# Kernel optimization log

Measured on AMD Instinct MI355X. Metric: run time of the kernel, lower is better.

The kernel has to match this reference:

```python
import jax, jax.numpy as jnp
import numpy as np

B, S, H, NH = 8, 1024, 1024, 16
HD = H // NH  # head dim = 64

def setup_inputs() -> dict:
    key = jax.random.key(0)
    ks = jax.random.split(key, 7)
    sc = 0.02
    return {
        "activation": jax.random.normal(ks[0], (B, S, H), jnp.float32),
        "qw": jax.random.normal(ks[1], (H, H), jnp.float32) * sc,
        "qb": jax.random.normal(ks[2], (H,), jnp.float32) * sc,
        "kw": jax.random.normal(ks[3], (H, H), jnp.float32) * sc,
        "kb": jax.random.normal(ks[4], (H,), jnp.float32) * sc,
        "vw": jax.random.normal(ks[5], (H, H), jnp.float32) * sc,
        "vb": jax.random.normal(ks[6], (H,), jnp.float32) * sc,
    }

def reference(activation, qw, qb, kw, kb, vw, vb):
    # QKV projections (torch Linear: x @ W^T + b)
    def proj(x, w, b):
        y = jnp.einsum('bsh,oh->bso', x, w) + b
        # split heads: [B,S,H] -> [B,NH,S,HD]
        return y.reshape(B, S, NH, HD).transpose(0, 2, 1, 3)
    q = proj(activation, qw, qb)
    k = proj(activation, kw, kb)
    v = proj(activation, vw, vb)
    # NOTE: source scales by 1/sqrt(hidden_dim), NOT 1/sqrt(head_dim)
    scale = 1.0 / jnp.sqrt(jnp.float32(H))
    scores = jnp.einsum('bnqd,bnkd->bnqk', q, k) * scale
    probs = jax.nn.softmax(scores, axis=-1)
    ctx = jnp.einsum('bnqk,bnkd->bnqd', probs, v)
    # merge heads: [B,NH,S,HD] -> [B,S,H]
    return ctx.transpose(0, 2, 1, 3).reshape(B, S, H)
```

## Files before the change

### kernel.cpp

```cpp
#include <hip/hip_runtime.h>
#include <cstdint>
#include <cstddef>

#define B_   8
#define S_   1024
#define H_   1024
#define NH_  16
#define HD_  64
#define M_   8192
#define N3_  3072
#define K_   1024

typedef __attribute__((ext_vector_type(8))) short bf16x8;
typedef __attribute__((ext_vector_type(4))) float f32x4;
typedef __attribute__((ext_vector_type(16))) float f32x16;
typedef __attribute__((ext_vector_type(8))) unsigned short u16x8;
typedef __attribute__((ext_vector_type(4))) unsigned u32x4;

__device__ __forceinline__ unsigned short f2bf(float f) {
  unsigned u = __builtin_bit_cast(unsigned, f);
  u += 0x7fffu + ((u >> 16) & 1u);
  return (unsigned short)(u >> 16);
}

__device__ __forceinline__ unsigned long long pack4bf(float a, float b,
                                                      float c, float d) {
  return (unsigned long long)f2bf(a)
       | ((unsigned long long)f2bf(b) << 16)
       | ((unsigned long long)f2bf(c) << 32)
       | ((unsigned long long)f2bf(d) << 48);
}

__device__ __forceinline__ unsigned cvtpk(float a, float b) {
  unsigned r;
  asm("v_cvt_pk_bf16_f32 %0, %1, %2" : "=v"(r) : "v"(a), "v"(b));
  return r;
}

__global__ void cvt_kernel(const float* __restrict__ src,
                           unsigned short* __restrict__ dst, int n) {
  const int stride = gridDim.x * blockDim.x * 8;
  for (int i = (blockIdx.x * blockDim.x + threadIdx.x) * 8; i < n; i += stride) {
    float4 a = *reinterpret_cast<const float4*>(src + i);
    float4 b = *reinterpret_cast<const float4*>(src + i + 4);
    u16x8 o;
    o[0] = f2bf(a.x); o[1] = f2bf(a.y); o[2] = f2bf(a.z); o[3] = f2bf(a.w);
    o[4] = f2bf(b.x); o[5] = f2bf(b.y); o[6] = f2bf(b.z); o[7] = f2bf(b.w);
    *reinterpret_cast<u16x8*>(dst + i) = o;
  }
}

__global__ void wcvt_kernel(const float* __restrict__ q,
                            const float* __restrict__ k,
                            const float* __restrict__ v,
                            unsigned short* __restrict__ dst) {
  const int i = (blockIdx.x * blockDim.x + threadIdx.x) * 8;
  const float* src;
  int off;
  if (i < 1048576)      { src = q; off = i; }
  else if (i < 2097152) { src = k; off = i - 1048576; }
  else                  { src = v; off = i - 2097152; }
  float4 a = *reinterpret_cast<const float4*>(src + off);
  float4 b = *reinterpret_cast<const float4*>(src + off + 4);
  u16x8 o;
  o[0] = f2bf(a.x); o[1] = f2bf(a.y); o[2] = f2bf(a.z); o[3] = f2bf(a.w);
  o[4] = f2bf(b.x); o[5] = f2bf(b.y); o[6] = f2bf(b.z); o[7] = f2bf(b.w);
  *reinterpret_cast<u16x8*>(dst + i) = o;
}

__global__ __launch_bounds__(256, 2) void qkv_gemm(
    const unsigned short* __restrict__ A,
    const unsigned short* __restrict__ Bw,
    const float* __restrict__ qb, const float* __restrict__ kb,
    const float* __restrict__ vb,
    unsigned short* __restrict__ Qh,
    unsigned short* __restrict__ Kh,
    unsigned short* __restrict__ Vth)
{
  extern __shared__ char sm[];
  const int t = threadIdx.x;
  const int lane = t & 63;
  const int wm = t >> 7, wn = (t >> 6) & 1;

  const int bid = blockIdx.x;
  const int c = bid >> 3;
  const int g = c >> 6;
  const int m = (c >> 3) & 7;
  const int n = c & 7;
  const int bm = (bid & 7) * 8 + m;
  const int bn = g * 8 + n;

  const char* Ab = (const char*)A + (size_t)bm * 128 * 2048;
  const char* Bb = (const char*)Bw + (size_t)bn * 128 * 2048;

  f32x4 acc[4][4] = {};

  #define STG(kt, buf)                                                         \
    { char* Ld = sm + (buf) * 32768;                                           \
      _Pragma("unroll")                                                        \
      for (int i = 0; i < 4; ++i) {                                            \
        const int off = (i * 256 + t) * 16;                                    \
        const int row = off >> 7;                                              \
        const int sc  = ((off >> 4) & 7) ^ (row & 7);                          \
        __builtin_amdgcn_global_load_lds(                                      \
          (const __attribute__((address_space(1))) void*)(Ab + (size_t)row * 2048 + (kt) * 128 + sc * 16), \
          (__attribute__((address_space(3))) void*)(Ld + off), 16, 0, 0);      \
        __builtin_amdgcn_global_load_lds(                                      \
          (const __attribute__((address_space(1))) void*)(Bb + (size_t)row * 2048 + (kt) * 128 + sc * 16), \
          (__attribute__((address_space(3))) void*)(Ld + 16384 + off), 16, 0, 0); \
      } }

  STG(0, 0)
  __syncthreads();

  for (int kt = 0; kt < 16; ++kt) {
    if (kt < 15) STG(kt + 1, (kt + 1) & 1)
    const char* Acur = sm + (kt & 1) * 32768;
    const char* Bcur = Acur + 16384;
    #pragma unroll
    for (int kk = 0; kk < 2; ++kk) {
      bf16x8 af[4], bf[4];
      #pragma unroll
      for (int mb = 0; mb < 4; ++mb) {
        const int row = wm * 64 + mb * 16 + (lane & 15);
        const int j   = kk * 4 + (lane >> 4);
        af[mb] = *(const bf16x8*)(Acur + row * 128 + ((j ^ (row & 7)) << 4));
      }
      #pragma unroll
      for (int nb = 0; nb < 4; ++nb) {
        const int row = wn * 64 + nb * 16 + (lane & 15);
        const int j   = kk * 4 + (lane >> 4);
        bf[nb] = *(const bf16x8*)(Bcur + row * 128 + ((j ^ (row & 7)) << 4));
      }
      __builtin_amdgcn_s_setprio(1);
      #pragma unroll
      for (int mb = 0; mb < 4; ++mb)
        #pragma unroll
        for (int nb = 0; nb < 4; ++nb)
          acc[mb][nb] = __builtin_amdgcn_mfma_f32_16x16x32_bf16(
              af[mb], bf[nb], acc[mb][nb], 0, 0, 0);
      __builtin_amdgcn_s_setprio(0);
    }
    __syncthreads();
  }

  const int tensor = bn >> 3;
  const float scl = (tensor == 0) ? 0.04508422f : 1.0f;
  const float* bias = (tensor == 0) ? qb : (tensor == 1) ? kb : vb;
  char* E = sm;
  const int bloc = bm >> 3;
  const int srow = (bm & 7) * 128;

  if (tensor < 2) {
    #pragma unroll
    for (int nb = 0; nb < 4; ++nb) {
      const int col = wn * 64 + nb * 16 + (lane & 15);
      const float bv = bias[(bn & 7) * 128 + col];
      #pragma unroll
      for (int mb = 0; mb < 4; ++mb) {
        #pragma unroll
        for (int r = 0; r < 4; ++r) {
          const int row = wm * 64 + mb * 16 + (lane >> 4) * 4 + r;
          const int byo = row * 256 + ((((col >> 3) ^ (row & 7)) << 4) | ((col & 7) << 1));
          *(unsigned short*)(E + byo) = f2bf((acc[mb][nb][r] + bv) * scl);
        }
      }
    }
    __syncthreads();
    unsigned short* dst = (tensor == 0) ? Qh : Kh;
    #pragma unroll
    for (int cch = 0; cch < 8; ++cch) {
      const int o = t * 128 + cch * 16;
      const int row = o >> 8;
      const int colb = o & 255;
      const int col = colb >> 1;
      u32x4 v = *(const u32x4*)(E + row * 256 + ((((colb >> 4) ^ (row & 7)) << 4)));
      const int sg = srow + row;
      const int nhh = (bn & 7) * 2 + (col >> 6);
      const size_t db = ((size_t)(bloc * NH_ + nhh) * S_ + sg) * 128 + (col & 63) * 2;
      *(u32x4*)((char*)dst + db) = v;
    }
  } else {
    #pragma unroll
    for (int nb = 0; nb < 4; ++nb) {
      const int col = wn * 64 + nb * 16 + (lane & 15);
      const float bv = bias[(bn & 7) * 128 + col];
      #pragma unroll
      for (int mb = 0; mb < 4; ++mb) {
        const int row0 = wm * 64 + mb * 16 + (lane >> 4) * 4;
        unsigned long long w = pack4bf(acc[mb][nb][0] + bv, acc[mb][nb][1] + bv,
                                       acc[mb][nb][2] + bv, acc[mb][nb][3] + bv);
        const int byo = col * 256 + ((((row0 >> 3) ^ (col & 7)) << 4) | ((row0 & 7) << 1));
        *(unsigned long long*)(E + byo) = w;
      }
    }
    __syncthreads();
    #pragma unroll
    for (int cch = 0; cch < 8; ++cch) {
      const int o = t * 128 + cch * 16;
      const int col = o >> 8;
      const int rowb = o & 255;
      const int row0 = rowb >> 1;
      u32x4 v = *(const u32x4*)(E + col * 256 + ((((rowb >> 4) ^ (col & 7)) << 4)));
      const int sg0 = srow + row0;
      const int nhh = (bn & 7) * 2 + (col >> 6);
      const size_t db = (size_t)(bloc * NH_ + nhh) * 131072 +
                        (size_t)(sg0 >> 6) * 8192 + (col & 63) * 128 + (sg0 & 63) * 2;
      *(u32x4*)((char*)Vth + db) = v;
    }
  }
}

__device__ __forceinline__ bf16x8 mk_frag(const f32x16& s, const int base) {
  unsigned a0 = cvtpk(s[base + 0], s[base + 1]);
  unsigned a1 = cvtpk(s[base + 2], s[base + 3]);
  unsigned b0 = cvtpk(s[base + 4], s[base + 5]);
  unsigned b1 = cvtpk(s[base + 6], s[base + 7]);
  asm("v_permlane32_swap_b32 %0, %1" : "+v"(a0), "+v"(b0));
  asm("v_permlane32_swap_b32 %0, %1" : "+v"(a1), "+v"(b1));
  u32x4 u = {a0, a1, b0, b1};
  return __builtin_bit_cast(bf16x8, u);
}

__global__ __launch_bounds__(256, 3) void attn_kernel(
    const unsigned short* __restrict__ Qh,
    const unsigned short* __restrict__ Kh,
    const unsigned short* __restrict__ Vth,
    float* __restrict__ Out)
{
  __shared__ char smx[2][16384];
  const int t = threadIdx.x;
  const int lane = t & 63;
  const int wave = t >> 6;
  const int l31 = lane & 31;
  const int hi = lane >> 5;
  const int hw = blockIdx.x;
  const int xcd = hw & 7;
  const int qt = (hw >> 3) & 7;
  const int bh = (hw >> 6) * 8 + xcd;
  const int b = bh >> 4, nh = bh & 15;

  const unsigned short* Qp = Qh + (size_t)bh * (S_ * HD_);
  const char* Kp = (const char*)Kh + (size_t)bh * 131072;
  const char* Vp = (const char*)Vth + (size_t)bh * 131072;
  const int q0 = qt * 128 + wave * 32;

  bf16x8 bq[4];
  #pragma unroll
  for (int st = 0; st < 4; ++st)
    bq[st] = *reinterpret_cast<const bf16x8*>(
        Qp + (size_t)(q0 + l31) * HD_ + st * 16 + hi * 8);

  const int soff0 = wave * 1024 + lane * 16;
  #define STAGE_TILE(dstbase, srcbase)                                            \
    _Pragma("unroll")                                                             \
    for (int j = 0; j < 2; ++j) {                                                 \
      const int off = j * 4096 + soff0;                                           \
      const int row = off >> 7;                                                   \
      const int sc  = ((off >> 4) & 7) ^ (row & 7);                               \
      __builtin_amdgcn_global_load_lds(                                           \
          (const __attribute__((address_space(1))) void*)((srcbase) + row * 128 + sc * 16), \
          (__attribute__((address_space(3))) void*)((dstbase) + off), 16, 0, 0);  \
    }

  STAGE_TILE(&smx[0][0],    Kp)
  STAGE_TILE(&smx[0][8192], Vp)
  __syncthreads();

  f32x16 o0 = {}, o1 = {};
  float lsum = 0.f;
  const int swr = l31 & 7;

  for (int kt = 0; kt < 16; ++kt) {
    const int cur = kt & 1;
    if (kt < 15) {
      STAGE_TILE(&smx[cur ^ 1][0],    Kp + (kt + 1) * 8192)
      STAGE_TILE(&smx[cur ^ 1][8192], Vp + (kt + 1) * 8192)
    }
    const char* Kb = &smx[cur][0];
    const char* Vb = &smx[cur][8192];

    f32x16 s0 = {}, s1 = {};
    #pragma unroll
    for (int st = 0; st < 4; ++st) {
      const int c = ((st * 2 + hi) ^ swr) << 4;
      bf16x8 ka = *reinterpret_cast<const bf16x8*>(Kb + l31 * 128 + c);
      bf16x8 kc = *reinterpret_cast<const bf16x8*>(Kb + (l31 + 32) * 128 + c);
      s0 = __builtin_amdgcn_mfma_f32_32x32x16_bf16(ka, bq[st], s0, 0, 0, 0);
      s1 = __builtin_amdgcn_mfma_f32_32x32x16_bf16(kc, bq[st], s1, 0, 0, 0);
    }

    bf16x8 va[4];
    #pragma unroll
    for (int ks = 0; ks < 2; ++ks) {
      const int c = ((ks * 2 + hi) ^ swr) << 4;
      va[ks * 2]     = *reinterpret_cast<const bf16x8*>(Vb + l31 * 128 + c);
      va[ks * 2 + 1] = *reinterpret_cast<const bf16x8*>(Vb + (l31 + 32) * 128 + c);
    }
    #pragma unroll
    for (int r = 0; r < 16; ++r) {
      s0[r] = __builtin_amdgcn_exp2f(s0[r]);
      lsum += s0[r];
    }
    bf16x8 f0 = mk_frag(s0, 0);
    bf16x8 f1 = mk_frag(s0, 8);
    o0 = __builtin_amdgcn_mfma_f32_32x32x16_bf16(f0, va[0], o0, 0, 0, 0);
    o1 = __builtin_amdgcn_mfma_f32_32x32x16_bf16(f0, va[1], o1, 0, 0, 0);
    o0 = __builtin_amdgcn_mfma_f32_32x32x16_bf16(f1, va[2], o0, 0, 0, 0);
    o1 = __builtin_amdgcn_mfma_f32_32x32x16_bf16(f1, va[3], o1, 0, 0, 0);

    #pragma unroll
    for (int ks = 0; ks < 2; ++ks) {
      const int c = (((ks + 2) * 2 + hi) ^ swr) << 4;
      va[ks * 2]     = *reinterpret_cast<const bf16x8*>(Vb + l31 * 128 + c);
      va[ks * 2 + 1] = *reinterpret_cast<const bf16x8*>(Vb + (l31 + 32) * 128 + c);
    }
    #pragma unroll
    for (int r = 0; r < 16; ++r) {
      s1[r] = __builtin_amdgcn_exp2f(s1[r]);
      lsum += s1[r];
    }
    bf16x8 f2 = mk_frag(s1, 0);
    bf16x8 f3 = mk_frag(s1, 8);
    o0 = __builtin_amdgcn_mfma_f32_32x32x16_bf16(f2, va[0], o0, 0, 0, 0);
    o1 = __builtin_amdgcn_mfma_f32_32x32x16_bf16(f2, va[1], o1, 0, 0, 0);
    o0 = __builtin_amdgcn_mfma_f32_32x32x16_bf16(f3, va[2], o0, 0, 0, 0);
    o1 = __builtin_amdgcn_mfma_f32_32x32x16_bf16(f3, va[3], o1, 0, 0, 0);

    __syncthreads();
  }

  const float ltot = lsum + __shfl_xor(lsum, 32);
  const float inv = 1.0f / ltot;
  #pragma unroll
  for (int r = 0; r < 16; ++r) {
    const int crow = (r & 3) + 8 * (r >> 2) + 4 * hi;
    const float invq = __shfl(inv, crow);
    float* op = Out + ((size_t)(b * S_ + q0 + crow)) * H_ + nh * HD_ + l31;
    op[0]  = o0[r] * invq;
    op[32] = o1[r] * invq;
  }
}

extern "C" void kernel_launch(void* const* d_in, const int* in_sizes, int n_in,
                              void* d_out, int out_size, void* d_ws, size_t ws_size,
                              hipStream_t stream) {
  const float* act = (const float*)d_in[0];
  const float* qw  = (const float*)d_in[1];
  const float* qb  = (const float*)d_in[2];
  const float* kw  = (const float*)d_in[3];
  const float* kb  = (const float*)d_in[4];
  const float* vw  = (const float*)d_in[5];
  const float* vb  = (const float*)d_in[6];

  char* ws = (char*)d_ws;
  unsigned short* actb = (unsigned short*)ws;
  unsigned short* wb   = (unsigned short*)(ws + 16777216);
  unsigned short* Qh   = (unsigned short*)(ws + 23068672);
  unsigned short* Kh   = Qh + 8388608;
  unsigned short* Vth  = Kh + 8388608;

  cvt_kernel<<<4096, 256, 0, stream>>>(act, actb, M_ * K_);
  wcvt_kernel<<<1536, 256, 0, stream>>>(qw, kw, vw, wb);

  hipFuncSetAttribute((const void*)qkv_gemm,
                      hipFuncAttributeMaxDynamicSharedMemorySize, 65536);
  qkv_gemm<<<1536, 256, 65536, stream>>>(actb, wb, qb, kb, vb, Qh, Kh, Vth);

  attn_kernel<<<1024, 256, 0, stream>>>(Qh, Kh, Vth, (float*)d_out);
}
```

Before: 122.7 us.

## Enlarge QKV GEMM tile to 256x128 with 512 threads and triple-buffered LDS

The QKV projection GEMM now runs 8 waves per block on a 256x128 output tile instead of 4 waves on 128x128. This halves the block count and improves reuse of the weight tile loaded into LDS. The main loop switches to a three-stage LDS ring, 144 KB in total, with two tiles prefetched ahead. A and B loads are issued in separate k-phases and synchronised with explicit vmcnt waits and raw barriers instead of __syncthreads. The epilogue indexing is adapted to the taller tile. The cost is one block per CU, so latency hiding depends on the hand-written pipeline rather than on occupancy.

Measured after the change: 129.9 us. 5.8% more time.

```diff
diff --git a/kernel.cpp b/kernel.cpp
--- a/kernel.cpp
+++ b/kernel.cpp
@@ -68,7 +68,7 @@
   *reinterpret_cast<u16x8*>(dst + i) = o;
 }
 
-__global__ __launch_bounds__(256, 2) void qkv_gemm(
+__global__ __launch_bounds__(512, 1) void qkv_gemm(
     const unsigned short* __restrict__ A,
     const unsigned short* __restrict__ Bw,
     const float* __restrict__ qb, const float* __restrict__ kb,
@@ -80,76 +80,107 @@
   extern __shared__ char sm[];
   const int t = threadIdx.x;
   const int lane = t & 63;
-  const int wm = t >> 7, wn = (t >> 6) & 1;
+  const int wave = t >> 6;
+  const int wm = wave >> 1;
+  const int wn = wave & 1;
 
   const int bid = blockIdx.x;
   const int c = bid >> 3;
-  const int g = c >> 6;
-  const int m = (c >> 3) & 7;
+  const int g = c >> 5;
+  const int m = (c >> 3) & 3;
   const int n = c & 7;
-  const int bm = (bid & 7) * 8 + m;
+  const int bm = (bid & 7) * 4 + m;
   const int bn = g * 8 + n;
 
-  const char* Ab = (const char*)A + (size_t)bm * 128 * 2048;
+  const char* Ab = (const char*)A + (size_t)bm * 256 * 2048;
   const char* Bb = (const char*)Bw + (size_t)bn * 128 * 2048;
 
   f32x4 acc[4][4] = {};
 
-  #define STG(kt, buf)                                                         \
-    { char* Ld = sm + (buf) * 32768;                                           \
+  #define STGA(kt, q, h)                                                       \
+    { char* Ld = sm + (q) * 49152 + (h) * 16384;                               \
       _Pragma("unroll")                                                        \
-      for (int i = 0; i < 4; ++i) {                                            \
-        const int off = (i * 256 + t) * 16;                                    \
-        const int row = off >> 7;                                              \
+      for (int j = 0; j < 2; ++j) {                                            \
+        const int off = j * 8192 + t * 16;                                     \
+        const int row = (h) * 128 + (off >> 7);                                \
         const int sc  = ((off >> 4) & 7) ^ (row & 7);                          \
         __builtin_amdgcn_global_load_lds(                                      \
           (const __attribute__((address_space(1))) void*)(Ab + (size_t)row * 2048 + (kt) * 128 + sc * 16), \
           (__attribute__((address_space(3))) void*)(Ld + off), 16, 0, 0);      \
+      } }
+  #define STGB(kt, q)                                                          \
+    { char* Ld = sm + (q) * 49152 + 32768;                                     \
+      _Pragma("unroll")                                                        \
+      for (int j = 0; j < 2; ++j) {                                            \
+        const int off = j * 8192 + t * 16;                                     \
+        const int row = off >> 7;                                              \
+        const int sc  = ((off >> 4) & 7) ^ (row & 7);                          \
         __builtin_amdgcn_global_load_lds(                                      \
           (const __attribute__((address_space(1))) void*)(Bb + (size_t)row * 2048 + (kt) * 128 + sc * 16), \
-          (__attribute__((address_space(3))) void*)(Ld + 16384 + off), 16, 0, 0); \
+          (__attribute__((address_space(3))) void*)(Ld + off), 16, 0, 0);      \
       } }
 
-  STG(0, 0)
+  #define VM6 asm volatile("s_waitcnt vmcnt(6)" ::: "memory")
+  #define VM0 asm volatile("s_waitcnt vmcnt(0)" ::: "memory")
+  #define BARR asm volatile("s_barrier" ::: "memory")
+
+  #define PH_READS(KK)                                                         \
+    bf16x8 af[4], bf[4];                                                       \
+    _Pragma("unroll")                                                          \
+    for (int mb = 0; mb < 4; ++mb) {                                           \
+      const int row = wm * 64 + mb * 16 + (lane & 15);                         \
+      af[mb] = *(const bf16x8*)(Acur + row * 128 +                             \
+                ((((KK) * 4 + (lane >> 4)) ^ (row & 7)) << 4));                \
+    }                                                                          \
+    _Pragma("unroll")                                                          \
+    for (int nb = 0; nb < 4; ++nb) {                                           \
+      const int row = wn * 64 + nb * 16 + (lane & 15);                         \
+      bf[nb] = *(const bf16x8*)(Bcur + row * 128 +                             \
+                ((((KK) * 4 + (lane >> 4)) ^ (row & 7)) << 4));                \
+    }
+  #define PH_MFMA                                                              \
+    __builtin_amdgcn_s_setprio(1);                                             \
+    _Pragma("unroll")                                                          \
+    for (int mb = 0; mb < 4; ++mb)                                             \
+      _Pragma("unroll")                                                        \
+      for (int nb = 0; nb < 4; ++nb)                                           \
+        acc[mb][nb] = __builtin_amdgcn_mfma_f32_16x16x32_bf16(                 \
+            af[mb], bf[nb], acc[mb][nb], 0, 0, 0);                             \
+    __builtin_amdgcn_s_setprio(0);
+
+  STGA(0, 0, 0) STGA(0, 0, 1) STGB(0, 0)
+  STGA(1, 1, 0) STGA(1, 1, 1) STGB(1, 1)
+  VM6;
+  BARR;
+
+  for (int kt = 0; kt < 16; ++kt) {
+    const char* Acur = sm + (kt % 3) * 49152;
+    const char* Bcur = Acur + 32768;
+    const int qn = (kt + 2) % 3;
+    {
+      PH_READS(0)
+      if (kt < 14) { STGA(kt + 2, qn, 0) STGA(kt + 2, qn, 1) }
+      BARR;
+      PH_MFMA
+      BARR;
+    }
+    {
+      PH_READS(1)
+      if (kt < 14) { STGB(kt + 2, qn) VM6; }
+      else if (kt == 14) VM0;
+      BARR;
+      PH_MFMA
+      BARR;
+    }
+  }
   __syncthreads();
-
-  for (int kt = 0; kt < 16; ++kt) {
-    if (kt < 15) STG(kt + 1, (kt + 1) & 1)
-    const char* Acur = sm + (kt & 1) * 32768;
-    const char* Bcur = Acur + 16384;
-    #pragma unroll
-    for (int kk = 0; kk < 2; ++kk) {
-      bf16x8 af[4], bf[4];
-      #pragma unroll
-      for (int mb = 0; mb < 4; ++mb) {
-        const int row = wm * 64 + mb * 16 + (lane & 15);
-        const int j   = kk * 4 + (lane >> 4);
-        af[mb] = *(const bf16x8*)(Acur + row * 128 + ((j ^ (row & 7)) << 4));
-      }
-      #pragma unroll
-      for (int nb = 0; nb < 4; ++nb) {
-        const int row = wn * 64 + nb * 16 + (lane & 15);
-        const int j   = kk * 4 + (lane >> 4);
-        bf[nb] = *(const bf16x8*)(Bcur + row * 128 + ((j ^ (row & 7)) << 4));
-      }
-      __builtin_amdgcn_s_setprio(1);
-      #pragma unroll
-      for (int mb = 0; mb < 4; ++mb)
-        #pragma unroll
-        for (int nb = 0; nb < 4; ++nb)
-          acc[mb][nb] = __builtin_amdgcn_mfma_f32_16x16x32_bf16(
-              af[mb], bf[nb], acc[mb][nb], 0, 0, 0);
-      __builtin_amdgcn_s_setprio(0);
-    }
-    __syncthreads();
-  }
 
   const int tensor = bn >> 3;
   const float scl = (tensor == 0) ? 0.04508422f : 1.0f;
   const float* bias = (tensor == 0) ? qb : (tensor == 1) ? kb : vb;
   char* E = sm;
-  const int bloc = bm >> 3;
-  const int srow = (bm & 7) * 128;
+  const int bloc = bm >> 2;
+  const int srow = (bm & 3) * 256;
 
   if (tensor < 2) {
     #pragma unroll
@@ -177,7 +208,7 @@
       u32x4 v = *(const u32x4*)(E + row * 256 + ((((colb >> 4) ^ (row & 7)) << 4)));
       const int sg = srow + row;
       const int nhh = (bn & 7) * 2 + (col >> 6);
-      const size_t db = ((size_t)(bloc * NH_ + nhh) * S_ + sg) * 128 + (col & 63) * 2;
+      const size_t db = ((size_t)(bloc * NH_ + nhh) * S_ + (sg & 1023)) * 128 + (col & 63) * 2;
       *(u32x4*)((char*)dst + db) = v;
     }
   } else {
@@ -190,7 +221,7 @@
         const int row0 = wm * 64 + mb * 16 + (lane >> 4) * 4;
         unsigned long long w = pack4bf(acc[mb][nb][0] + bv, acc[mb][nb][1] + bv,
                                        acc[mb][nb][2] + bv, acc[mb][nb][3] + bv);
-        const int byo = col * 256 + ((((row0 >> 3) ^ (col & 7)) << 4) | ((row0 & 7) << 1));
+        const int byo = col * 512 + ((((row0 >> 3) ^ (col & 7)) << 4) | ((row0 & 7) << 1));
         *(unsigned long long*)(E + byo) = w;
       }
     }
@@ -198,14 +229,14 @@
     #pragma unroll
     for (int cch = 0; cch < 8; ++cch) {
       const int o = t * 128 + cch * 16;
-      const int col = o >> 8;
-      const int rowb = o & 255;
+      const int col = o >> 9;
+      const int rowb = o & 511;
       const int row0 = rowb >> 1;
-      u32x4 v = *(const u32x4*)(E + col * 256 + ((((rowb >> 4) ^ (col & 7)) << 4)));
+      u32x4 v = *(const u32x4*)(E + col * 512 + ((((rowb >> 4) ^ (col & 7)) << 4)));
       const int sg0 = srow + row0;
       const int nhh = (bn & 7) * 2 + (col >> 6);
       const size_t db = (size_t)(bloc * NH_ + nhh) * 131072 +
-                        (size_t)(sg0 >> 6) * 8192 + (col & 63) * 128 + (sg0 & 63) * 2;
+                        (size_t)((sg0 & 1023) >> 6) * 8192 + (col & 63) * 128 + (sg0 & 63) * 2;
       *(u32x4*)((char*)Vth + db) = v;
     }
   }
@@ -364,8 +395,8 @@
   wcvt_kernel<<<1536, 256, 0, stream>>>(qw, kw, vw, wb);
 
   hipFuncSetAttribute((const void*)qkv_gemm,
-                      hipFuncAttributeMaxDynamicSharedMemorySize, 65536);
-  qkv_gemm<<<1536, 256, 65536, stream>>>(actb, wb, qb, kb, vb, Qh, Kh, Vth);
+                      hipFuncAttributeMaxDynamicSharedMemorySize, 147456);
+  qkv_gemm<<<768, 512, 147456, stream>>>(actb, wb, qb, kb, vb, Qh, Kh, Vth);
 
   attn_kernel<<<1024, 256, 0, stream>>>(Qh, Kh, Vth, (float*)d_out);
 }
```
